# Kernel optimization log

Hardware: AMD Instinct MI355X
Metric: run time of the kernel (lower is better)

## Reference

```python
import jax, jax.numpy as jnp
import numpy as np

H = 32        # num attention heads
KVH = 8       # num key/value heads
HD = 64       # head dim
D = H * HD    # hidden size 2048
EPS = 1e-6
ROPE_THETA = 10000.0
MAX_POS = 2048


def rotate_half(x):
    x1, x2 = jnp.split(x, 2, axis=-1)
    return jnp.concatenate((-x2, x1), axis=-1)


def rms_norm(x, w):
    # per-head RMSNorm over last dim, computed in fp32 like the torch module
    x32 = x.astype(jnp.float32)
    inv = jax.lax.rsqrt(jnp.mean(x32 * x32, axis=-1, keepdims=True) + EPS)
    return w * (x32 * inv).astype(x.dtype)


def setup_inputs() -> dict:
    key = jax.random.key(0)
    ks = jax.random.split(key, 6)
    B, S = 2, 2048
    hidden_states = jax.random.normal(ks[0], (B, S, D), dtype=jnp.float32)
    # rotary tables [MAX_POS, HD]
    inv_freq = 1.0 / (ROPE_THETA ** (np.arange(0, HD, 2, dtype=np.float32) / HD))
    t = np.arange(MAX_POS, dtype=np.float32)
    freqs = np.outer(t, inv_freq)                      # [MAX_POS, HD/2]
    emb = np.concatenate([freqs, freqs], axis=-1)      # [MAX_POS, HD]
    cos = jnp.asarray(np.cos(emb))
    sin = jnp.asarray(np.sin(emb))
    scale = 1.0 / np.sqrt(D)
    wq = jax.random.normal(ks[1], (D, D), dtype=jnp.float32) * scale
    wk = jax.random.normal(ks[2], (D, KVH * HD), dtype=jnp.float32) * scale
    wv = jax.random.normal(ks[3], (D, KVH * HD), dtype=jnp.float32) * scale
    wo = jax.random.normal(ks[4], (D, D), dtype=jnp.float32) * scale
    q_ln_w = jnp.ones((HD,), dtype=jnp.float32)
    k_ln_w = jnp.ones((HD,), dtype=jnp.float32)
    return {"hidden_states": hidden_states, "cos": cos, "sin": sin,
            "wq": wq, "wk": wk, "wv": wv, "wo": wo,
            "q_ln_w": q_ln_w, "k_ln_w": k_ln_w}


def reference(hidden_states, cos, sin, wq, wk, wv, wo, q_ln_w, k_ln_w):
    B, S, _ = hidden_states.shape
    n_rep = H // KVH
    q = (hidden_states @ wq).reshape(B, S, H, HD)
    k = (hidden_states @ wk).reshape(B, S, KVH, HD)
    v = (hidden_states @ wv).reshape(B, S, KVH, HD)
    # per-head RMSNorm on q/k, then to (B, heads, S, HD)
    q = rms_norm(q, q_ln_w).transpose(0, 2, 1, 3)
    k = rms_norm(k, k_ln_w).transpose(0, 2, 1, 3)
    v = v.transpose(0, 2, 1, 3)
    # RoPE
    c = cos[:S][None, None]  # [1,1,S,HD]
    s = sin[:S][None, None]
    q = q * c + rotate_half(q) * s
    k = k * c + rotate_half(k) * s
    # GQA: repeat kv heads
    k = jnp.repeat(k, n_rep, axis=1)
    v = jnp.repeat(v, n_rep, axis=1)
    scores = jnp.einsum('bhqd,bhkd->bhqk', q, k) / np.sqrt(HD)
    causal = jnp.tril(jnp.ones((S, S), dtype=bool))
    scores = jnp.where(causal, scores, -jnp.inf)
    p = jax.nn.softmax(scores.astype(jnp.float32), axis=-1).astype(q.dtype)
    out = jnp.einsum('bhqk,bhkd->bhqd', p, v)
    out = out.transpose(0, 2, 1, 3).reshape(B, S, D)
    return out @ wo
```

## Files before the change

### kernel.cpp

```cpp
#include <hip/hip_runtime.h>
#include <hip/hip_bf16.h>

#define HH 32
#define KVHN 8
#define HD 64
#define DMODEL 2048
#define SEQ 2048
#define BB 2
#define NTOK 4096
#define DKV 512
#define NQKV 3072

typedef __bf16 bf16x8 __attribute__((ext_vector_type(8)));
typedef __bf16 bf16x4 __attribute__((ext_vector_type(4)));
typedef float  f32x4  __attribute__((ext_vector_type(4)));

typedef const __attribute__((address_space(1))) void gvoid_t;
typedef __attribute__((address_space(3))) void lvoid_t;

__device__ inline void glds16(const void* g, void* l) {
  __builtin_amdgcn_global_load_lds((gvoid_t*)g, (lvoid_t*)l, 16, 0, 0);
}

__device__ inline f32x4 mfma16(bf16x8 a, bf16x8 b, f32x4 c) {
  return __builtin_amdgcn_mfma_f32_16x16x32_bf16(a, b, c, 0, 0, 0);
}

__device__ inline float fast_exp2(float x) {
  float r;
  asm("v_exp_f32 %0, %1" : "=v"(r) : "v"(x));
  return r;
}


__global__ __launch_bounds__(256)
void k_cvt_hidden(const float* __restrict__ in, __bf16* __restrict__ out) {
  int i = (blockIdx.x * 256 + threadIdx.x) * 4;
  f32x4 v = *(const f32x4*)(in + i);
  bf16x4 o;
  o[0] = (__bf16)v[0]; o[1] = (__bf16)v[1]; o[2] = (__bf16)v[2]; o[3] = (__bf16)v[3];
  *(bf16x4*)(out + i) = o;
}

__global__ __launch_bounds__(256)
void k_transpose_w(const float* __restrict__ W, __bf16* __restrict__ T, int K, int N) {
  __shared__ float tile[32][33];
  int n0 = blockIdx.x * 32, k0 = blockIdx.y * 32;
  int tx = threadIdx.x & 31, ty = threadIdx.x >> 5;
#pragma unroll
  for (int i = 0; i < 32; i += 8)
    tile[ty + i][tx] = W[(size_t)(k0 + ty + i) * N + n0 + tx];
  __syncthreads();
#pragma unroll
  for (int i = 0; i < 32; i += 8)
    T[(size_t)(n0 + ty + i) * K + k0 + tx] = (__bf16)tile[tx][ty + i];
}

__global__ __launch_bounds__(256)
void k_transpose_kv(const float* __restrict__ WK, const float* __restrict__ WV,
                    __bf16* __restrict__ T) {
  __shared__ float tile[32][33];
  const float* W = blockIdx.z ? WV : WK;
  __bf16* Td = T + (size_t)(2048 + blockIdx.z * 512) * 2048;
  int n0 = blockIdx.x * 32, k0 = blockIdx.y * 32;
  int tx = threadIdx.x & 31, ty = threadIdx.x >> 5;
#pragma unroll
  for (int i = 0; i < 32; i += 8)
    tile[ty + i][tx] = W[(size_t)(k0 + ty + i) * 512 + n0 + tx];
  __syncthreads();
#pragma unroll
  for (int i = 0; i < 32; i += 8)
    Td[(size_t)(n0 + ty + i) * 2048 + k0 + tx] = (__bf16)tile[tx][ty + i];
}

__global__ __launch_bounds__(256)
void k_transpose_v(const __bf16* __restrict__ Vt, __bf16* __restrict__ VT) {
  __shared__ __bf16 tile[32][33];
  int c0 = blockIdx.x * 32, s0 = blockIdx.y * 32, b = blockIdx.z;
  int tx = threadIdx.x & 31, ty = threadIdx.x >> 5;
#pragma unroll
  for (int i = 0; i < 32; i += 8)
    tile[ty + i][tx] = Vt[(size_t)(b * SEQ + s0 + ty + i) * DKV + c0 + tx];
  __syncthreads();
#pragma unroll
  for (int i = 0; i < 32; i += 8)
    VT[(size_t)(b * DKV + c0 + ty + i) * SEQ + s0 + tx] = tile[tx][ty + i];
}


__device__ inline void stc(float* p, float v)  { *p = v; }
__device__ inline void stc(__bf16* p, float v) { *p = (__bf16)v; }

template <int EPI, typename CT>
__global__ __launch_bounds__(256, 4)
void k_gemm3(const __bf16* __restrict__ A, const __bf16* __restrict__ BT,
             CT* __restrict__ C, int M, int N, int K,
             const float* __restrict__ cosT, const float* __restrict__ sinT,
             const float* __restrict__ qw, const float* __restrict__ kw,
             __bf16* __restrict__ Qr, __bf16* __restrict__ Kr,
             __bf16* __restrict__ Vt) {
  __shared__ alignas(16) __bf16 Al[2][128 * 32];
  __shared__ alignas(16) __bf16 Bl[2][128 * 32];
  const int tid = threadIdx.x;
  const int wid = tid >> 6, lane = tid & 63, g = lane >> 4, r16 = lane & 15;
  const int wm = wid >> 1, wn = wid & 1;
  const int nbm = M >> 7, nbn = N >> 7;
  const int nwg = nbm * nbn;
  int id = blockIdx.x;
  id = (id & 7) * (nwg >> 3) + (id >> 3);
  const int bm = id % nbm, bn = id / nbm;

  const int pp = tid >> 3;
  const int c8 = (tid & 7) ^ (pp & 7);
  const int sr1 = 2 * pp + (c8 >> 2);
  const int sr2 = 64 + sr1;
  const int c1 = (c8 & 3) * 8;
  const __bf16* gA1 = A + (size_t)(bm * 128 + sr1) * K + c1;
  const __bf16* gA2 = A + (size_t)(bm * 128 + sr2) * K + c1;
  const __bf16* gB1 = BT + (size_t)(bn * 128 + sr1) * K + c1;
  const __bf16* gB2 = BT + (size_t)(bn * 128 + sr2) * K + c1;

  int aoff[4], boff[4];
#pragma unroll
  for (int m = 0; m < 4; ++m) {
    int row = wm * 64 + m * 16 + r16;
    aoff[m] = (row >> 1) * 64 + (((((row & 1) << 2) | g) ^ ((row >> 1) & 7)) * 8);
  }
#pragma unroll
  for (int n = 0; n < 4; ++n) {
    int row = wn * 64 + n * 16 + r16;
    boff[n] = (row >> 1) * 64 + (((((row & 1) << 2) | g) ^ ((row >> 1) & 7)) * 8);
  }

  auto STAGE = [&](int sl, int kt) {
    const int ko = kt * 32;
    glds16(gA1 + ko, &Al[sl][tid * 8]);
    glds16(gA2 + ko, &Al[sl][2048 + tid * 8]);
    glds16(gB1 + ko, &Bl[sl][tid * 8]);
    glds16(gB2 + ko, &Bl[sl][2048 + tid * 8]);
  };

  f32x4 acc[4][4] = {};
  const int nk = K >> 5;

  STAGE(0, 0);
  for (int kt = 0; kt < nk; ++kt) {
    const int s = kt & 1;
    if (kt + 1 < nk) {
      STAGE(s ^ 1, kt + 1);
      asm volatile("s_waitcnt vmcnt(4)" ::: "memory");
    } else {
      asm volatile("s_waitcnt vmcnt(0)" ::: "memory");
    }
    __builtin_amdgcn_s_barrier();
    bf16x8 af[4], bfr[4];
#pragma unroll
    for (int m = 0; m < 4; ++m) af[m] = *(const bf16x8*)&Al[s][aoff[m]];
#pragma unroll
    for (int n = 0; n < 4; ++n) bfr[n] = *(const bf16x8*)&Bl[s][boff[n]];
    __builtin_amdgcn_s_setprio(1);
#pragma unroll
    for (int m = 0; m < 4; ++m)
#pragma unroll
      for (int n = 0; n < 4; ++n)
        acc[m][n] = mfma16(af[m], bfr[n], acc[m][n]);
    __builtin_amdgcn_s_setprio(0);
    __builtin_amdgcn_s_barrier();
  }

  if (EPI == 0) {
#pragma unroll
    for (int m = 0; m < 4; ++m) {
      int row = bm * 128 + wm * 64 + m * 16 + g * 4;
#pragma unroll
      for (int n = 0; n < 4; ++n) {
        int col = bn * 128 + wn * 64 + n * 16 + r16;
#pragma unroll
        for (int r = 0; r < 4; ++r)
          stc(&C[(size_t)(row + r) * N + col], acc[m][n][r]);
      }
    }
  } else {
    const int colbase = bn * 128 + wn * 64;
    const float QSCALE = 0.18033688011112042f;
    if (colbase < DMODEL + DKV) {
      const bool isq = colbase < DMODEL;
      const float* wp = isq ? qw : kw;
      const float qs = isq ? QSCALE : 1.0f;
      float w4[4];
#pragma unroll
      for (int n = 0; n < 4; ++n) w4[n] = wp[n * 16 + r16];
#pragma unroll
      for (int m = 0; m < 4; ++m) {
        const int rowm = bm * 128 + wm * 64 + m * 16 + g * 4;
        float ss[4];
#pragma unroll
        for (int r = 0; r < 4; ++r) {
          ss[r] = acc[m][0][r] * acc[m][0][r] + acc[m][1][r] * acc[m][1][r] +
                  acc[m][2][r] * acc[m][2][r] + acc[m][3][r] * acc[m][3][r];
#pragma unroll
          for (int mk = 1; mk < 16; mk <<= 1) ss[r] += __shfl_xor(ss[r], mk);
          ss[r] = rsqrtf(ss[r] * (1.0f / HD) + 1e-6f);
        }
#pragma unroll
        for (int r = 0; r < 4; ++r) {
          const int t = rowm + r;
          const int sidx = t & (SEQ - 1);
          const float inv_ = ss[r];
#pragma unroll
          for (int n = 0; n < 4; ++n) {
            const int d = n * 16 + r16;
            const float xn = acc[m][n][r] * inv_ * w4[n];
            const float xp = acc[m][n ^ 2][r] * inv_ * w4[n ^ 2];
            const float rot = (n < 2) ? -xp : xp;
            const float cv = cosT[sidx * HD + d], sv = sinT[sidx * HD + d];
            const float o = (xn * cv + rot * sv) * qs;
            if (isq) {
              const int hq = colbase >> 6;
              Qr[((size_t)t * HH + hq) * HD + d] = (__bf16)o;
            } else {
              const int kvh = (colbase - DMODEL) >> 6;
              Kr[((size_t)t * KVHN + kvh) * HD + d] = (__bf16)o;
            }
          }
        }
      }
    } else {
      const int vc0 = colbase - (DMODEL + DKV);
#pragma unroll
      for (int m = 0; m < 4; ++m) {
        const int rowm = bm * 128 + wm * 64 + m * 16 + g * 4;
#pragma unroll
        for (int n = 0; n < 4; ++n)
#pragma unroll
          for (int r = 0; r < 4; ++r)
            Vt[(size_t)(rowm + r) * DKV + vc0 + n * 16 + r16] = (__bf16)acc[m][n][r];
      }
    }
  }
}


__global__ __launch_bounds__(512)
void k_attn(const __bf16* __restrict__ Q, const __bf16* __restrict__ Kg,
            const __bf16* __restrict__ VT, __bf16* __restrict__ O) {
  __shared__ alignas(16) __bf16 Kl[2][64 * 64];
  __shared__ alignas(16) __bf16 Vl[2][64 * 64];
  __shared__ alignas(16) __bf16 Pl[8][16 * 72];
  const int f = blockIdx.x;
  const int b = f >> 8;
  const int h = (f & 255) >> 3;
  const int j = f & 7;
  const int kvh = h >> 2;
  const int tid = threadIdx.x, wid = tid >> 6, lane = tid & 63;
  const int g = lane >> 4, r16 = lane & 15;
  __bf16* Pw = Pl[wid];

  const int rr = lane >> 3;
  const int cc = (lane & 7) ^ rr;

  auto STAGE = [&](int buf, int kb) {
    const int krow = kb * 64 + wid * 8 + rr;
    glds16(&Kg[((size_t)(b * SEQ + krow) * KVHN + kvh) * HD + cc * 8],
           &Kl[buf][wid * 512]);
    const int d = wid * 8 + rr;
    glds16(&VT[(size_t)(b * DKV + kvh * HD + d) * SEQ + (size_t)kb * 64 + cc * 8],
           &Vl[buf][wid * 512]);
  };

#pragma unroll 1
  for (int phase = 0; phase < 2; ++phase) {
    const int qt = phase ? j : 15 - j;
    const int q0 = qt * 128 + wid * 16;
    const int ntile = 2 * qt + 2;

    bf16x8 qf[2];
#pragma unroll
    for (int h2 = 0; h2 < 2; ++h2)
      qf[h2] = *(const bf16x8*)&Q[(((size_t)b * SEQ + q0 + r16) * HH + h) * HD + h2 * 32 + g * 8];

    f32x4 acc[4] = {};
    float l_q = 0.0f;

    STAGE(0, 0);
    asm volatile("s_waitcnt vmcnt(0)" ::: "memory");
    __syncthreads();

    for (int kb = 0; kb < ntile; ++kb) {
      const int cur = kb & 1;
      if (kb + 1 < ntile) STAGE(cur ^ 1, kb + 1);
      const __bf16* Kb = Kl[cur];
      const __bf16* Vb = Vl[cur];
      if (kb * 64 <= q0 + 15) {
        bf16x8 kf[4][2];
#pragma unroll
        for (int ks = 0; ks < 4; ++ks)
#pragma unroll
          for (int h2 = 0; h2 < 2; ++h2) {
            const int p = r16 + ks * 16;
            const int ch = (g + 4 * h2) ^ (p & 7);
            kf[ks][h2] = *(const bf16x8*)&Kb[p * 64 + ch * 8];
          }
        const bool needmask = (kb * 64 + 63 > q0);
        float svv[4][4];
        __builtin_amdgcn_s_setprio(1);
#pragma unroll
        for (int ks = 0; ks < 4; ++ks) {
          f32x4 sacc = {-12.f, -12.f, -12.f, -12.f};
          sacc = mfma16(kf[ks][0], qf[0], sacc);
          sacc = mfma16(kf[ks][1], qf[1], sacc);
#pragma unroll
          for (int r = 0; r < 4; ++r) svv[ks][r] = sacc[r];
        }
        __builtin_amdgcn_s_setprio(0);
        if (needmask) {
#pragma unroll
          for (int ks = 0; ks < 4; ++ks)
#pragma unroll
            for (int r = 0; r < 4; ++r) {
              int pg = kb * 64 + ks * 16 + g * 4 + r;
              int qg = q0 + r16;
              if (pg > qg) svv[ks][r] = -1e30f;
            }
        }
#pragma unroll
        for (int ks = 0; ks < 4; ++ks) {
          bf16x4 pk;
#pragma unroll
          for (int r = 0; r < 4; ++r) {
            float p = fast_exp2(svv[ks][r]);
            l_q += p;
            pk[r] = (__bf16)p;
          }
          *(bf16x4*)&Pw[r16 * 72 + ks * 16 + g * 4] = pk;
        }
        bf16x8 pf0 = *(const bf16x8*)&Pw[r16 * 72 + g * 8];
        bf16x8 pf1 = *(const bf16x8*)&Pw[r16 * 72 + 32 + g * 8];
        __builtin_amdgcn_s_setprio(1);
#pragma unroll
        for (int nb = 0; nb < 4; ++nb) {
          const int d = r16 + nb * 16;
          const int ch0 = g ^ (d & 7), ch1 = (4 + g) ^ (d & 7);
          bf16x8 vf0 = *(const bf16x8*)&Vb[d * 64 + ch0 * 8];
          bf16x8 vf1 = *(const bf16x8*)&Vb[d * 64 + ch1 * 8];
          acc[nb] = mfma16(pf0, vf0, acc[nb]);
          acc[nb] = mfma16(pf1, vf1, acc[nb]);
        }
        __builtin_amdgcn_s_setprio(0);
      }
      asm volatile("s_waitcnt vmcnt(0)" ::: "memory");
      __syncthreads();
    }
    l_q += __shfl_xor(l_q, 16);
    l_q += __shfl_xor(l_q, 32);
    const float invq = 1.0f / l_q;
    float inv[4];
#pragma unroll
    for (int r = 0; r < 4; ++r) inv[r] = __shfl(invq, g * 4 + r);
#pragma unroll
    for (int nb = 0; nb < 4; ++nb)
#pragma unroll
      for (int r = 0; r < 4; ++r)
        O[(((size_t)b * SEQ + q0 + g * 4 + r) * HH + h) * HD + nb * 16 + r16] =
            (__bf16)(acc[nb][r] * inv[r]);
  }
}


extern "C" void kernel_launch(void* const* d_in, const int* in_sizes, int n_in,
                              void* d_out, int out_size, void* d_ws, size_t ws_size,
                              hipStream_t stream) {
  const float* hidden = (const float*)d_in[0];
  const float* cosT   = (const float*)d_in[1];
  const float* sinT   = (const float*)d_in[2];
  const float* wq     = (const float*)d_in[3];
  const float* wk     = (const float*)d_in[4];
  const float* wv     = (const float*)d_in[5];
  const float* wo     = (const float*)d_in[6];
  const float* qw     = (const float*)d_in[7];
  const float* kw     = (const float*)d_in[8];
  float* out = (float*)d_out;
  char* ws = (char*)d_ws;

  __bf16* Abf  = (__bf16*)(ws);
  __bf16* Ob   = Abf;
  __bf16* WT   = (__bf16*)(ws + (16u << 20));
  __bf16* Qr   = (__bf16*)(ws + (28u << 20));
  __bf16* Kr   = (__bf16*)(ws + (44u << 20));
  __bf16* Vtmp = (__bf16*)(ws + (48u << 20));
  __bf16* VT   = (__bf16*)(ws + (52u << 20));
  __bf16* WoT  = (__bf16*)(ws + (56u << 20));

  k_cvt_hidden<<<8192, 256, 0, stream>>>(hidden, Abf);
  k_transpose_w<<<dim3(64, 64), 256, 0, stream>>>(wq, WT, 2048, 2048);
  k_transpose_kv<<<dim3(16, 64, 2), 256, 0, stream>>>(wk, wv, WT);
  k_transpose_w<<<dim3(64, 64), 256, 0, stream>>>(wo, WoT, 2048, 2048);

  k_gemm3<1, __bf16><<<768, 256, 0, stream>>>(Abf, WT, (__bf16*)nullptr,
      NTOK, NQKV, DMODEL, cosT, sinT, qw, kw, Qr, Kr, Vtmp);

  k_transpose_v<<<dim3(16, 64, 2), 256, 0, stream>>>(Vtmp, VT);

  k_attn<<<dim3(512), 512, 0, stream>>>(Qr, Kr, VT, Ob);

  k_gemm3<0, float><<<512, 256, 0, stream>>>(Ob, WoT, out,
      NTOK, DMODEL, DMODEL, nullptr, nullptr, nullptr, nullptr,
      nullptr, nullptr, nullptr);
}
```

Measured before the change: 194.3 us.

## Merge prep kernels into one launch and write V transposed from QKV GEMM

Combines the hidden-state conversion and three weight-transpose kernels into a single k_prep launch that dispatches on block index. The QKV GEMM epilogue now writes V directly in the transposed [b, kv-channel, seq] layout with 4-wide bf16 stores, which removes the separate V transpose kernel and its intermediate buffer. This cuts launch overhead and an extra global round trip, but the transposed V stores are strided by SEQ across lanes and so coalesce less well than before.

Result: faster. 186.2 us (median of 2 runs) (-4.2%).

```diff
diff --git a/kernel.cpp b/kernel.cpp
--- a/kernel.cpp
+++ b/kernel.cpp
@@ -34,19 +34,35 @@
 
 
 __global__ __launch_bounds__(256)
-void k_cvt_hidden(const float* __restrict__ in, __bf16* __restrict__ out) {
-  int i = (blockIdx.x * 256 + threadIdx.x) * 4;
-  f32x4 v = *(const f32x4*)(in + i);
-  bf16x4 o;
-  o[0] = (__bf16)v[0]; o[1] = (__bf16)v[1]; o[2] = (__bf16)v[2]; o[3] = (__bf16)v[3];
-  *(bf16x4*)(out + i) = o;
-}
-
-__global__ __launch_bounds__(256)
-void k_transpose_w(const float* __restrict__ W, __bf16* __restrict__ T, int K, int N) {
+void k_prep(const float* __restrict__ hidden, __bf16* __restrict__ Abf,
+            const float* __restrict__ wq, const float* __restrict__ wk,
+            const float* __restrict__ wv, const float* __restrict__ wo,
+            __bf16* __restrict__ WT, __bf16* __restrict__ WoT) {
   __shared__ float tile[32][33];
-  int n0 = blockIdx.x * 32, k0 = blockIdx.y * 32;
-  int tx = threadIdx.x & 31, ty = threadIdx.x >> 5;
+  const int id = blockIdx.x, tid = threadIdx.x;
+  if (id < 8192) {
+    int i = (id * 256 + tid) * 4;
+    f32x4 v = *(const f32x4*)(hidden + i);
+    bf16x4 o;
+    o[0] = (__bf16)v[0]; o[1] = (__bf16)v[1];
+    o[2] = (__bf16)v[2]; o[3] = (__bf16)v[3];
+    *(bf16x4*)(Abf + i) = o;
+    return;
+  }
+  const float* W; __bf16* T; int K, N, n0, k0;
+  if (id < 12288) {
+    int t = id - 8192; W = wq; T = WT; K = 2048; N = 2048;
+    n0 = (t & 63) * 32; k0 = (t >> 6) * 32;
+  } else if (id < 14336) {
+    int t = id - 12288; int z = t >> 10;
+    W = z ? wv : wk; T = WT + (size_t)(2048 + z * 512) * 2048;
+    K = 2048; N = 512;
+    n0 = (t & 15) * 32; k0 = ((t >> 4) & 63) * 32;
+  } else {
+    int t = id - 14336; W = wo; T = WoT; K = 2048; N = 2048;
+    n0 = (t & 63) * 32; k0 = (t >> 6) * 32;
+  }
+  int tx = tid & 31, ty = tid >> 5;
 #pragma unroll
   for (int i = 0; i < 32; i += 8)
     tile[ty + i][tx] = W[(size_t)(k0 + ty + i) * N + n0 + tx];
@@ -54,37 +70,6 @@
 #pragma unroll
   for (int i = 0; i < 32; i += 8)
     T[(size_t)(n0 + ty + i) * K + k0 + tx] = (__bf16)tile[tx][ty + i];
-}
-
-__global__ __launch_bounds__(256)
-void k_transpose_kv(const float* __restrict__ WK, const float* __restrict__ WV,
-                    __bf16* __restrict__ T) {
-  __shared__ float tile[32][33];
-  const float* W = blockIdx.z ? WV : WK;
-  __bf16* Td = T + (size_t)(2048 + blockIdx.z * 512) * 2048;
-  int n0 = blockIdx.x * 32, k0 = blockIdx.y * 32;
-  int tx = threadIdx.x & 31, ty = threadIdx.x >> 5;
-#pragma unroll
-  for (int i = 0; i < 32; i += 8)
-    tile[ty + i][tx] = W[(size_t)(k0 + ty + i) * 512 + n0 + tx];
-  __syncthreads();
-#pragma unroll
-  for (int i = 0; i < 32; i += 8)
-    Td[(size_t)(n0 + ty + i) * 2048 + k0 + tx] = (__bf16)tile[tx][ty + i];
-}
-
-__global__ __launch_bounds__(256)
-void k_transpose_v(const __bf16* __restrict__ Vt, __bf16* __restrict__ VT) {
-  __shared__ __bf16 tile[32][33];
-  int c0 = blockIdx.x * 32, s0 = blockIdx.y * 32, b = blockIdx.z;
-  int tx = threadIdx.x & 31, ty = threadIdx.x >> 5;
-#pragma unroll
-  for (int i = 0; i < 32; i += 8)
-    tile[ty + i][tx] = Vt[(size_t)(b * SEQ + s0 + ty + i) * DKV + c0 + tx];
-  __syncthreads();
-#pragma unroll
-  for (int i = 0; i < 32; i += 8)
-    VT[(size_t)(b * DKV + c0 + ty + i) * SEQ + s0 + tx] = tile[tx][ty + i];
 }
 
 
@@ -230,11 +215,16 @@
 #pragma unroll
       for (int m = 0; m < 4; ++m) {
         const int rowm = bm * 128 + wm * 64 + m * 16 + g * 4;
-#pragma unroll
-        for (int n = 0; n < 4; ++n)
-#pragma unroll
-          for (int r = 0; r < 4; ++r)
-            Vt[(size_t)(rowm + r) * DKV + vc0 + n * 16 + r16] = (__bf16)acc[m][n][r];
+        const int bb2 = rowm >> 11;
+        const int s0 = rowm & (SEQ - 1);
+#pragma unroll
+        for (int n = 0; n < 4; ++n) {
+          const int c = vc0 + n * 16 + r16;
+          bf16x4 pk;
+#pragma unroll
+          for (int r = 0; r < 4; ++r) pk[r] = (__bf16)acc[m][n][r];
+          *(bf16x4*)&Vt[((size_t)bb2 * DKV + c) * SEQ + s0] = pk;
+        }
       }
     }
   }
@@ -387,19 +377,13 @@
   __bf16* WT   = (__bf16*)(ws + (16u << 20));
   __bf16* Qr   = (__bf16*)(ws + (28u << 20));
   __bf16* Kr   = (__bf16*)(ws + (44u << 20));
-  __bf16* Vtmp = (__bf16*)(ws + (48u << 20));
   __bf16* VT   = (__bf16*)(ws + (52u << 20));
   __bf16* WoT  = (__bf16*)(ws + (56u << 20));
 
-  k_cvt_hidden<<<8192, 256, 0, stream>>>(hidden, Abf);
-  k_transpose_w<<<dim3(64, 64), 256, 0, stream>>>(wq, WT, 2048, 2048);
-  k_transpose_kv<<<dim3(16, 64, 2), 256, 0, stream>>>(wk, wv, WT);
-  k_transpose_w<<<dim3(64, 64), 256, 0, stream>>>(wo, WoT, 2048, 2048);
+  k_prep<<<18432, 256, 0, stream>>>(hidden, Abf, wq, wk, wv, wo, WT, WoT);
 
   k_gemm3<1, __bf16><<<768, 256, 0, stream>>>(Abf, WT, (__bf16*)nullptr,
-      NTOK, NQKV, DMODEL, cosT, sinT, qw, kw, Qr, Kr, Vtmp);
-
-  k_transpose_v<<<dim3(16, 64, 2), 256, 0, stream>>>(Vtmp, VT);
+      NTOK, NQKV, DMODEL, cosT, sinT, qw, kw, Qr, Kr, VT);
 
   k_attn<<<dim3(512), 512, 0, stream>>>(Qr, Kr, VT, Ob);
 
```
